# Performance work log

Measured on AMD Instinct MI355X. Metric: run time of the kernel, lower is better.

The kernel has to match this reference:

```python
import jax, jax.numpy as jnp
import numpy as np

B, S, H, NH = 4, 4096, 1024, 16
HD = H // NH  # head_dim = 64


def setup_inputs() -> dict:
    key = jax.random.key(0)
    ks = jax.random.split(key, 8)
    scale = 0.02
    return {
        "hidden_states": jax.random.normal(ks[0], (B, S, H), dtype=jnp.float32),
        "attention_mask": jnp.ones((B, S), dtype=jnp.float32),
        "Wq": jax.random.normal(ks[1], (H, H), dtype=jnp.float32) * scale,
        "bq": jnp.zeros((H,), dtype=jnp.float32),
        "Wk": jax.random.normal(ks[2], (H, H), dtype=jnp.float32) * scale,
        "bk": jnp.zeros((H,), dtype=jnp.float32),
        "Wv": jax.random.normal(ks[3], (H, H), dtype=jnp.float32) * scale,
        "bv": jnp.zeros((H,), dtype=jnp.float32),
        "Wo": jax.random.normal(ks[4], (H, H), dtype=jnp.float32) * scale,
        "bo": jnp.zeros((H,), dtype=jnp.float32),
    }


def _heads(x):
    # [B,S,H] -> [B,NH,S,HD]
    b, s, _ = x.shape
    return x.reshape(b, s, NH, HD).transpose(0, 2, 1, 3)


def reference(hidden_states, attention_mask, Wq, bq, Wk, bk, Wv, bv, Wo, bo):
    b, s, _ = hidden_states.shape
    q = _heads(hidden_states @ Wq.T + bq)
    k = _heads(hidden_states @ Wk.T + bk)
    v = _heads(hidden_states @ Wv.T + bv)

    m = attention_mask[:, None, :, None]  # [B,1,S,1]
    k = k * m
    v = v * m

    # Faithful to the torch code: kv_i = matmul(k_i[b,h,1,d], v_i[b,h,d,1])
    # is the SCALAR dot product k_t . v_t, broadcast-added to the [d,d] state.
    # => state_t = (cumsum_t k_t.v_t) * ones(d,d)
    # => o_t = state_t @ q_t = (cumsum_t k_t.v_t) * sum_j q_t[j], same for every i.
    dots = jnp.einsum('bhsd,bhsd->bhs', k, v)        # scalar k.v per step
    cum = jnp.cumsum(dots, axis=-1)                  # running state scalar
    qsum = jnp.sum(q, axis=-1)                       # [B,NH,S]
    o = jnp.broadcast_to((cum * qsum)[..., None], q.shape)  # [B,NH,S,HD]

    out = o.transpose(0, 2, 1, 3).reshape(b, s, NH * HD)
    out = out @ Wo.T + bo  # dropout is identity (eval / p handled as 0)

    # final state: last cumulative scalar broadcast over the [d,d] matrix
    state = jnp.broadcast_to(cum[:, :, -1, None, None], (b, NH, HD, HD))
    return out, state
```

## Files before the change

kernel.cpp:

```cpp
#include <hip/hip_runtime.h>


typedef __attribute__((ext_vector_type(4))) float f32x4;
typedef __attribute__((ext_vector_type(8))) short bf16x8;
typedef __attribute__((ext_vector_type(8))) unsigned short u16x8;
typedef unsigned int u32;

#define GLDS16(g, l)                                                            \
  __builtin_amdgcn_global_load_lds((const __attribute__((address_space(1))) u32*)(g), \
                                   (__attribute__((address_space(3))) u32*)(l), 16, 0, 0)
#define MFMA16(a, b, c) __builtin_amdgcn_mfma_f32_16x16x32_bf16(a, b, c, 0, 0, 0)

__device__ __forceinline__ unsigned short f2bf(float f) {
  union { float f; u32 u; } x; x.f = f;
  u32 r = (x.u + 0x7fffu + ((x.u >> 16) & 1u)) >> 16;
  return (unsigned short)r;
}

__global__ void k_prep(const float* __restrict__ X, unsigned short* __restrict__ Xb,
                       const float* __restrict__ Wq, const float* __restrict__ bq,
                       const float* __restrict__ Wk, const float* __restrict__ bk,
                       const float* __restrict__ Wv, const float* __restrict__ bv,
                       const float* __restrict__ Wo,
                       unsigned short* __restrict__ Wkb, unsigned short* __restrict__ Wvb,
                       unsigned short* __restrict__ SWb, float* __restrict__ WosT,
                       float* __restrict__ scal) {
  int blk = blockIdx.x, t = threadIdx.x;
  if (blk < 2048) {
    const float* src = (blk < 1024) ? Wk : Wv;
    unsigned short* dst = (blk < 1024) ? Wkb : Wvb;
    size_t i = ((size_t)(blk & 1023) * 256 + t) * 4;
    f32x4 v = *(const f32x4*)(src + i);
    dst[i + 0] = f2bf(v.x); dst[i + 1] = f2bf(v.y);
    dst[i + 2] = f2bf(v.z); dst[i + 3] = f2bf(v.w);
  } else if (blk < 2241) {
    int b2 = blk - 2048;
    if (b2 < 128) {
      int o = b2 * 256 + t;
      int r = o >> 10, c = o & 1023;
      float s = 0.f;
      if (r < 16) {
        for (int d = 0; d < 64; ++d) s += Wq[(size_t)(r * 64 + d) * 1024 + c];
      } else {
        int h = r - 16;
        for (int d = 0; d < 64; ++d) {
          int j = h * 64 + d;
          s += bv[j] * Wk[(size_t)j * 1024 + c] + bk[j] * Wv[(size_t)j * 1024 + c];
        }
      }
      SWb[o] = f2bf(s);
    } else if (b2 < 192) {
      int o = (b2 - 128) * 256 + t;
      int h = o >> 10, j = o & 1023;
      float s = 0.f;
      for (int d = 0; d < 64; ++d) s += Wo[(size_t)j * 1024 + h * 64 + d];
      WosT[o] = s;
    } else {
      if (t < 16) {
        float s = 0.f;
        for (int d = 0; d < 64; ++d) s += bq[t * 64 + d];
        scal[t] = s;
      } else if (t < 32) {
        int h = t - 16;
        float s = 0.f;
        for (int d = 0; d < 64; ++d) s += bk[h * 64 + d] * bv[h * 64 + d];
        scal[t] = s;
      }
    }
  } else {
    size_t i = ((size_t)(blk - 2241) * 256 + t) * 8;
    f32x4 a = *(const f32x4*)(X + i);
    f32x4 b = *(const f32x4*)(X + i + 4);
    u16x8 o;
    o[0] = f2bf(a.x); o[1] = f2bf(a.y); o[2] = f2bf(a.z); o[3] = f2bf(a.w);
    o[4] = f2bf(b.x); o[5] = f2bf(b.y); o[6] = f2bf(b.z); o[7] = f2bf(b.w);
    *(u16x8*)(Xb + i) = o;
  }
}

#define NT 32
__global__ __launch_bounds__(512, 2) void k_dualgemm(
    const unsigned short* __restrict__ Xb,
    const unsigned short* __restrict__ Wkb,
    const unsigned short* __restrict__ Wvb,
    float* __restrict__ dotsT) {
  extern __shared__ __align__(16) unsigned short lds[];
  int orig = blockIdx.x;
  int wg = (orig & 7) * 64 + (orig >> 3);
  int bx = wg & 7, by = wg >> 3;
  int row0 = by << 8, col0 = bx << 7;
  int tid = threadIdx.x, wid = tid >> 6, lane = tid & 63;
  int wrM = wid >> 1, wcN = wid & 1;
  int fr = lane & 15, fg = lane >> 4;

  int uA0 = tid, uA1 = tid + 512;
  const unsigned short* sA0 = Xb + (size_t)(row0 + (uA0 >> 2)) * 1024 + (((uA0 & 3) ^ ((uA0 >> 3) & 3)) << 3);
  const unsigned short* sA1 = Xb + (size_t)(row0 + (uA1 >> 2)) * 1024 + (((uA1 & 3) ^ ((uA1 >> 3) & 3)) << 3);
  const unsigned short* sK  = Wkb + (size_t)(col0 + (tid >> 2)) * 1024 + (((tid & 3) ^ ((tid >> 3) & 3)) << 3);
  const unsigned short* sV  = Wvb + (size_t)(col0 + (tid >> 2)) * 1024 + (((tid & 3) ^ ((tid >> 3) & 3)) << 3);
  int dA0 = wid << 9, dA1 = 4096 + (wid << 9);
  int dK = 8192 + (wid << 9), dV = 12288 + (wid << 9);

  int xsw = (fg ^ ((fr >> 1) & 3)) << 3;
  int aro = (wrM * 64 + fr) * 32 + xsw;
  int bro = (wcN * 64 + fr) * 32 + xsw;

  f32x4 ck[4][4] = {{0}}, cv[4][4] = {{0}};

#pragma unroll
  for (int p = 0; p < 3; ++p) {
    int bb = p * 16384, ko = p * 32;
    GLDS16(sA0 + ko, lds + bb + dA0);
    GLDS16(sK + ko, lds + bb + dK);
    GLDS16(sA1 + ko, lds + bb + dA1);
    GLDS16(sV + ko, lds + bb + dV);
  }

  for (int t = 0; t < NT; ++t) {
    int rb = (t & 3) << 14;
    if (t < NT - 3) { asm volatile("s_waitcnt vmcnt(8)" ::: "memory"); }
    else            { asm volatile("s_waitcnt vmcnt(0)" ::: "memory"); }
    __builtin_amdgcn_s_barrier();
    __builtin_amdgcn_sched_barrier(0);

    bf16x8 a[4], bk[4], bv[4];
#pragma unroll
    for (int mi = 0; mi < 4; ++mi) a[mi] = *(const bf16x8*)(lds + rb + aro + mi * 512);
#pragma unroll
    for (int ni = 0; ni < 2; ++ni) {
      bk[ni] = *(const bf16x8*)(lds + rb + 8192 + bro + ni * 512);
      bv[ni] = *(const bf16x8*)(lds + rb + 12288 + bro + ni * 512);
    }
    int t3 = t + 3;
    int bb = (t3 & 3) << 14, ko = t3 << 5;
    if (t3 < NT) {
      GLDS16(sA0 + ko, lds + bb + dA0);
      GLDS16(sK + ko, lds + bb + dK);
    }
    asm volatile("s_waitcnt lgkmcnt(0)" ::: "memory");
    __builtin_amdgcn_sched_barrier(0);
    __builtin_amdgcn_s_setprio(1);
#pragma unroll
    for (int mi = 0; mi < 4; ++mi)
#pragma unroll
      for (int ni = 0; ni < 2; ++ni) {
        ck[mi][ni] = MFMA16(a[mi], bk[ni], ck[mi][ni]);
        cv[mi][ni] = MFMA16(a[mi], bv[ni], cv[mi][ni]);
      }
    __builtin_amdgcn_s_setprio(0);

#pragma unroll
    for (int ni = 2; ni < 4; ++ni) {
      bk[ni] = *(const bf16x8*)(lds + rb + 8192 + bro + ni * 512);
      bv[ni] = *(const bf16x8*)(lds + rb + 12288 + bro + ni * 512);
    }
    if (t3 < NT) {
      GLDS16(sA1 + ko, lds + bb + dA1);
      GLDS16(sV + ko, lds + bb + dV);
    }
    asm volatile("s_waitcnt lgkmcnt(0)" ::: "memory");
    __builtin_amdgcn_sched_barrier(0);
    __builtin_amdgcn_s_setprio(1);
#pragma unroll
    for (int mi = 0; mi < 4; ++mi)
#pragma unroll
      for (int ni = 2; ni < 4; ++ni) {
        ck[mi][ni] = MFMA16(a[mi], bk[ni], ck[mi][ni]);
        cv[mi][ni] = MFMA16(a[mi], bv[ni], cv[mi][ni]);
      }
    __builtin_amdgcn_s_setprio(0);
  }

  float part[4][4];
#pragma unroll
  for (int mi = 0; mi < 4; ++mi)
#pragma unroll
    for (int q = 0; q < 4; ++q) {
      float s = 0.f;
#pragma unroll
      for (int ni = 0; ni < 4; ++ni) s += ck[mi][ni][q] * cv[mi][ni][q];
      part[mi][q] = s;
    }
#pragma unroll
  for (int r = 0; r < 4; ++r) {
#pragma unroll
    for (int mi = 0; mi < 4; ++mi)
#pragma unroll
      for (int q = 0; q < 4; ++q)
        part[mi][q] += __shfl_xor(part[mi][q], 1 << r, 64);
  }
  int h = bx * 2 + wcN;
  if (fr == 0) {
#pragma unroll
    for (int mi = 0; mi < 4; ++mi)
#pragma unroll
      for (int q = 0; q < 4; ++q)
        dotsT[(size_t)h * 16384 + row0 + wrM * 64 + mi * 16 + fg * 4 + q] = part[mi][q];
  }
}

__global__ __launch_bounds__(512) void k_side(const unsigned short* __restrict__ Xb,
                                              const unsigned short* __restrict__ SWb,
                                              float* __restrict__ side4) {
  __shared__ __align__(16) unsigned short As[8192];
  __shared__ __align__(16) unsigned short Ss[1024];
  int rowblk = blockIdx.x >> 2, ks = blockIdx.x & 3;
  int row0 = rowblk << 8;
  int tid = threadIdx.x, wid = tid >> 6, lane = tid & 63;
  int fr = lane & 15, fg = lane >> 4;
  int uA0 = tid, uA1 = tid + 512;
  const unsigned short* sA0 = Xb + (size_t)(row0 + (uA0 >> 2)) * 1024 + ks * 256 + (((uA0 & 3) ^ ((uA0 >> 3) & 3)) << 3);
  const unsigned short* sA1 = Xb + (size_t)(row0 + (uA1 >> 2)) * 1024 + ks * 256 + (((uA1 & 3) ^ ((uA1 >> 3) & 3)) << 3);
  int uS = ((wid & 1) << 6) + lane;
  const unsigned short* sS = SWb + (size_t)(uS >> 2) * 1024 + ks * 256 + (((uS & 3) ^ ((uS >> 3) & 3)) << 3);
  int xsw = (fg ^ ((fr >> 1) & 3)) << 3;
  int aro = (wid * 32 + fr) * 32 + xsw;
  int sro = fr * 32 + xsw;
  f32x4 acc[2][2] = {{0}};
  for (int t = 0; t < 8; ++t) {
    int ko = t << 5;
    __syncthreads();
    GLDS16(sA0 + ko, As + (wid << 9));
    GLDS16(sA1 + ko, As + 4096 + (wid << 9));
    GLDS16(sS + ko, Ss + ((wid & 1) << 9));
    __syncthreads();
    bf16x8 a0 = *(const bf16x8*)(As + aro);
    bf16x8 a1 = *(const bf16x8*)(As + aro + 512);
    bf16x8 s0 = *(const bf16x8*)(Ss + sro);
    bf16x8 s1 = *(const bf16x8*)(Ss + sro + 512);
    acc[0][0] = MFMA16(a0, s0, acc[0][0]);
    acc[0][1] = MFMA16(a0, s1, acc[0][1]);
    acc[1][0] = MFMA16(a1, s0, acc[1][0]);
    acc[1][1] = MFMA16(a1, s1, acc[1][1]);
  }
  size_t mbase = row0 + wid * 32;
#pragma unroll
  for (int mi = 0; mi < 2; ++mi)
#pragma unroll
    for (int ni = 0; ni < 2; ++ni)
#pragma unroll
      for (int q = 0; q < 4; ++q)
        side4[(size_t)((ni * 4 + ks) * 16 + fr) * 16384 + mbase + mi * 16 + fg * 4 + q] =
            acc[mi][ni][q];
}

__global__ void k_cumsum(const float* __restrict__ dotsT, const float* __restrict__ side4,
                         const float* __restrict__ scal, const float* __restrict__ mask,
                         float* __restrict__ coef, float* __restrict__ state) {
  __shared__ float csum[256];
  int b = blockIdx.x >> 4, h = blockIdx.x & 15;
  int t = threadIdx.x;
  float bqs = scal[h], dbc = scal[16 + h];
  size_t m0 = (size_t)b * 4096;
  const size_t KSS = (size_t)16 * 16384;
  const float* dro = dotsT + (size_t)h * 16384 + m0;
  const float* qb = side4 + (size_t)h * 16384 + m0;
  const float* db = side4 + 4 * KSS + (size_t)h * 16384 + m0;
  const float* mko = mask + m0;
  float loc[16], run = 0.f;
  int s0 = t * 16;
#pragma unroll
  for (int i = 0; i < 16; ++i) {
    int ii = s0 + i;
    float mk = mko[ii];
    float dball = db[ii] + db[ii + KSS] + db[ii + 2 * KSS] + db[ii + 3 * KSS];
    float d = (dro[ii] + dball + dbc) * mk * mk;
    run += d;
    loc[i] = run;
  }
  csum[t] = run;
  __syncthreads();
  for (int off = 1; off < 256; off <<= 1) {
    float v = (t >= off) ? csum[t - off] : 0.f;
    __syncthreads();
    csum[t] += v;
    __syncthreads();
  }
  float prefix = csum[t] - run;
#pragma unroll
  for (int i = 0; i < 16; ++i) {
    int ii = s0 + i;
    float cum = prefix + loc[i];
    float qs = qb[ii] + qb[ii + KSS] + qb[ii + 2 * KSS] + qb[ii + 3 * KSS];
    coef[(m0 + ii) * 16 + h] = cum * (qs + bqs);
  }
  float total = csum[255];
  float* sp = state + (size_t)(b * 16 + h) * 4096;
  for (int i = t; i < 4096; i += 256) sp[i] = total;
}

__global__ __launch_bounds__(256) void k_outgemm(const float* __restrict__ coef,
                                                 const float* __restrict__ WosT,
                                                 const float* __restrict__ bo,
                                                 float* __restrict__ out) {
  int t = threadIdx.x;
  int j0 = t * 4;
  f32x4 w4[16];
#pragma unroll
  for (int hh = 0; hh < 16; ++hh) w4[hh] = *(const f32x4*)&WosT[hh * 1024 + j0];
  f32x4 bov = *(const f32x4*)&bo[j0];
  size_t m0 = (size_t)blockIdx.x * 32;
  for (int mi = 0; mi < 32; ++mi) {
    size_t m = m0 + mi;
    const float* cm = &coef[m * 16];
    f32x4 acc = bov;
#pragma unroll
    for (int hh = 0; hh < 16; ++hh) acc += w4[hh] * cm[hh];
    *(f32x4*)&out[m * 1024 + j0] = acc;
  }
}

extern "C" void kernel_launch(void* const* d_in, const int* in_sizes, int n_in,
                              void* d_out, int out_size, void* d_ws, size_t ws_size,
                              hipStream_t stream) {
  const float* X    = (const float*)d_in[0];
  const float* mask = (const float*)d_in[1];
  const float* Wq   = (const float*)d_in[2];
  const float* bq   = (const float*)d_in[3];
  const float* Wk   = (const float*)d_in[4];
  const float* bk   = (const float*)d_in[5];
  const float* Wv   = (const float*)d_in[6];
  const float* bv   = (const float*)d_in[7];
  const float* Wo   = (const float*)d_in[8];
  const float* bo   = (const float*)d_in[9];
  float* out   = (float*)d_out;
  float* state = out + (size_t)16384 * 1024;

  char* w = (char*)d_ws;
  unsigned short* Xb  = (unsigned short*)w; w += (size_t)16384 * 1024 * 2;
  unsigned short* Wkb = (unsigned short*)w; w += (size_t)1024 * 1024 * 2;
  unsigned short* Wvb = (unsigned short*)w; w += (size_t)1024 * 1024 * 2;
  unsigned short* SWb = (unsigned short*)w; w += (size_t)32 * 1024 * 2;
  float* WosT  = (float*)w; w += (size_t)16 * 1024 * 4;
  float* scal  = (float*)w; w += 256;
  float* dotsT = (float*)w; w += (size_t)16 * 16384 * 4;
  float* side4 = (float*)w; w += (size_t)8 * 16 * 16384 * 4;
  float* coef  = (float*)w; w += (size_t)16384 * 16 * 4;

  (void)hipFuncSetAttribute((const void*)k_dualgemm,
                            hipFuncAttributeMaxDynamicSharedMemorySize, 131072);

  hipLaunchKernelGGL(k_prep,     dim3(10433), dim3(256), 0, stream,
                     X, Xb, Wq, bq, Wk, bk, Wv, bv, Wo, Wkb, Wvb, SWb, WosT, scal);
  hipLaunchKernelGGL(k_dualgemm, dim3(512),  dim3(512), 131072, stream, Xb, Wkb, Wvb, dotsT);
  hipLaunchKernelGGL(k_side,     dim3(256),  dim3(512), 0, stream, Xb, SWb, side4);
  hipLaunchKernelGGL(k_cumsum,   dim3(64),   dim3(256), 0, stream, dotsT, side4, scal,
                     mask, coef, state);
  hipLaunchKernelGGL(k_outgemm,  dim3(512),  dim3(256), 0, stream, coef, WosT, bo, out);
}
```

Measured before the change: 116.5 us.

## Merge side GEMM into dual-GEMM launch and split main loop into four phases

The separate k_side kernel is folded into k_dualgemm as 256 extra workgroups, which removes one launch and lets the side GEMM run alongside the main GEMM tail. The main K-loop is restructured into four phases (K-lo, V-lo, K-hi, V-hi), each issuing one global-to-LDS load and running its MFMAs between barriers. The goal is finer interleaving of loads with compute. The cost is many more barriers per iteration, and the side blocks now reserve 128KB of dynamic LDS, which can limit occupancy.

```diff
diff --git a/kernel.cpp b/kernel.cpp
--- a/kernel.cpp
+++ b/kernel.cpp
@@ -10,6 +10,9 @@
   __builtin_amdgcn_global_load_lds((const __attribute__((address_space(1))) u32*)(g), \
                                    (__attribute__((address_space(3))) u32*)(l), 16, 0, 0)
 #define MFMA16(a, b, c) __builtin_amdgcn_mfma_f32_16x16x32_bf16(a, b, c, 0, 0, 0)
+#define PH_BAR __builtin_amdgcn_s_barrier()
+#define LGK0 do { asm volatile("s_waitcnt lgkmcnt(0)" ::: "memory"); \
+                  __builtin_amdgcn_sched_barrier(0); } while (0)
 
 __device__ __forceinline__ unsigned short f2bf(float f) {
   union { float f; u32 u; } x; x.f = f;
@@ -83,15 +86,61 @@
     const unsigned short* __restrict__ Xb,
     const unsigned short* __restrict__ Wkb,
     const unsigned short* __restrict__ Wvb,
-    float* __restrict__ dotsT) {
+    const unsigned short* __restrict__ SWb,
+    float* __restrict__ dotsT, float* __restrict__ side4) {
   extern __shared__ __align__(16) unsigned short lds[];
   int orig = blockIdx.x;
+  int tid = threadIdx.x, wid = tid >> 6, lane = tid & 63;
+  int fr = lane & 15, fg = lane >> 4;
+
+  if (orig >= 512) {
+    int unit = orig - 512;
+    int rowblk = unit >> 2, ks = unit & 3;
+    int row0 = rowblk << 8;
+    unsigned short* As = lds;
+    unsigned short* Ss = lds + 8192;
+    int uA0 = tid, uA1 = tid + 512;
+    const unsigned short* sA0 = Xb + (size_t)(row0 + (uA0 >> 2)) * 1024 + ks * 256 + (((uA0 & 3) ^ ((uA0 >> 3) & 3)) << 3);
+    const unsigned short* sA1 = Xb + (size_t)(row0 + (uA1 >> 2)) * 1024 + ks * 256 + (((uA1 & 3) ^ ((uA1 >> 3) & 3)) << 3);
+    int uS = ((wid & 1) << 6) + lane;
+    const unsigned short* sS = SWb + (size_t)(uS >> 2) * 1024 + ks * 256 + (((uS & 3) ^ ((uS >> 3) & 3)) << 3);
+    int xsw = (fg ^ ((fr >> 1) & 3)) << 3;
+    int aro = (wid * 32 + fr) * 32 + xsw;
+    int sro = fr * 32 + xsw;
+    f32x4 acc[2][2] = {{0}};
+    for (int t = 0; t < 8; ++t) {
+      int ko = t << 5;
+      __syncthreads();
+      GLDS16(sA0 + ko, As + (wid << 9));
+      GLDS16(sA1 + ko, As + 4096 + (wid << 9));
+      GLDS16(sS + ko, Ss + ((wid & 1) << 9));
+      asm volatile("s_waitcnt vmcnt(0)" ::: "memory");
+      __syncthreads();
+      bf16x8 a0 = *(const bf16x8*)(As + aro);
+      bf16x8 a1 = *(const bf16x8*)(As + aro + 512);
+      bf16x8 s0 = *(const bf16x8*)(Ss + sro);
+      bf16x8 s1 = *(const bf16x8*)(Ss + sro + 512);
+      acc[0][0] = MFMA16(a0, s0, acc[0][0]);
+      acc[0][1] = MFMA16(a0, s1, acc[0][1]);
+      acc[1][0] = MFMA16(a1, s0, acc[1][0]);
+      acc[1][1] = MFMA16(a1, s1, acc[1][1]);
+    }
+    size_t mbase = row0 + wid * 32;
+#pragma unroll
+    for (int mi = 0; mi < 2; ++mi)
+#pragma unroll
+      for (int ni = 0; ni < 2; ++ni)
+#pragma unroll
+        for (int q = 0; q < 4; ++q)
+          side4[(size_t)((ni * 4 + ks) * 16 + fr) * 16384 + mbase + mi * 16 + fg * 4 + q] =
+              acc[mi][ni][q];
+    return;
+  }
+
   int wg = (orig & 7) * 64 + (orig >> 3);
   int bx = wg & 7, by = wg >> 3;
   int row0 = by << 8, col0 = bx << 7;
-  int tid = threadIdx.x, wid = tid >> 6, lane = tid & 63;
   int wrM = wid >> 1, wcN = wid & 1;
-  int fr = lane & 15, fg = lane >> 4;
 
   int uA0 = tid, uA1 = tid + 512;
   const unsigned short* sA0 = Xb + (size_t)(row0 + (uA0 >> 2)) * 1024 + (((uA0 & 3) ^ ((uA0 >> 3) & 3)) << 3);
@@ -115,60 +164,73 @@
     GLDS16(sA1 + ko, lds + bb + dA1);
     GLDS16(sV + ko, lds + bb + dV);
   }
+  asm volatile("s_waitcnt vmcnt(8)" ::: "memory");
+  PH_BAR;
 
   for (int t = 0; t < NT; ++t) {
-    int rb = (t & 3) << 14;
-    if (t < NT - 3) { asm volatile("s_waitcnt vmcnt(8)" ::: "memory"); }
-    else            { asm volatile("s_waitcnt vmcnt(0)" ::: "memory"); }
-    __builtin_amdgcn_s_barrier();
-    __builtin_amdgcn_sched_barrier(0);
-
+    const int rb = (t & 3) << 14;
+    const int t3 = t + 3;
+    const int bb = (t3 & 3) << 14;
+    const int ko = t3 << 5;
+    const bool st = (t3 < NT);
     bf16x8 a[4], bk[4], bv[4];
+
 #pragma unroll
     for (int mi = 0; mi < 4; ++mi) a[mi] = *(const bf16x8*)(lds + rb + aro + mi * 512);
-#pragma unroll
-    for (int ni = 0; ni < 2; ++ni) {
-      bk[ni] = *(const bf16x8*)(lds + rb + 8192 + bro + ni * 512);
-      bv[ni] = *(const bf16x8*)(lds + rb + 12288 + bro + ni * 512);
-    }
-    int t3 = t + 3;
-    int bb = (t3 & 3) << 14, ko = t3 << 5;
-    if (t3 < NT) {
-      GLDS16(sA0 + ko, lds + bb + dA0);
-      GLDS16(sK + ko, lds + bb + dK);
-    }
-    asm volatile("s_waitcnt lgkmcnt(0)" ::: "memory");
-    __builtin_amdgcn_sched_barrier(0);
+    bk[0] = *(const bf16x8*)(lds + rb + 8192 + bro);
+    bk[1] = *(const bf16x8*)(lds + rb + 8192 + bro + 512);
+    if (st) GLDS16(sA0 + ko, lds + bb + dA0);
+    PH_BAR; LGK0;
     __builtin_amdgcn_s_setprio(1);
 #pragma unroll
-    for (int mi = 0; mi < 4; ++mi)
-#pragma unroll
-      for (int ni = 0; ni < 2; ++ni) {
-        ck[mi][ni] = MFMA16(a[mi], bk[ni], ck[mi][ni]);
-        cv[mi][ni] = MFMA16(a[mi], bv[ni], cv[mi][ni]);
-      }
+    for (int mi = 0; mi < 4; ++mi) {
+      ck[mi][0] = MFMA16(a[mi], bk[0], ck[mi][0]);
+      ck[mi][1] = MFMA16(a[mi], bk[1], ck[mi][1]);
+    }
     __builtin_amdgcn_s_setprio(0);
-
-#pragma unroll
-    for (int ni = 2; ni < 4; ++ni) {
-      bk[ni] = *(const bf16x8*)(lds + rb + 8192 + bro + ni * 512);
-      bv[ni] = *(const bf16x8*)(lds + rb + 12288 + bro + ni * 512);
-    }
-    if (t3 < NT) {
-      GLDS16(sA1 + ko, lds + bb + dA1);
-      GLDS16(sV + ko, lds + bb + dV);
-    }
-    asm volatile("s_waitcnt lgkmcnt(0)" ::: "memory");
-    __builtin_amdgcn_sched_barrier(0);
+    PH_BAR;
+
+    bv[0] = *(const bf16x8*)(lds + rb + 12288 + bro);
+    bv[1] = *(const bf16x8*)(lds + rb + 12288 + bro + 512);
+    if (st) GLDS16(sK + ko, lds + bb + dK);
+    PH_BAR; LGK0;
     __builtin_amdgcn_s_setprio(1);
 #pragma unroll
-    for (int mi = 0; mi < 4; ++mi)
-#pragma unroll
-      for (int ni = 2; ni < 4; ++ni) {
-        ck[mi][ni] = MFMA16(a[mi], bk[ni], ck[mi][ni]);
-        cv[mi][ni] = MFMA16(a[mi], bv[ni], cv[mi][ni]);
-      }
+    for (int mi = 0; mi < 4; ++mi) {
+      cv[mi][0] = MFMA16(a[mi], bv[0], cv[mi][0]);
+      cv[mi][1] = MFMA16(a[mi], bv[1], cv[mi][1]);
+    }
     __builtin_amdgcn_s_setprio(0);
+    PH_BAR;
+
+    bk[2] = *(const bf16x8*)(lds + rb + 8192 + bro + 1024);
+    bk[3] = *(const bf16x8*)(lds + rb + 8192 + bro + 1536);
+    if (st) GLDS16(sA1 + ko, lds + bb + dA1);
+    PH_BAR; LGK0;
+    __builtin_amdgcn_s_setprio(1);
+#pragma unroll
+    for (int mi = 0; mi < 4; ++mi) {
+      ck[mi][2] = MFMA16(a[mi], bk[2], ck[mi][2]);
+      ck[mi][3] = MFMA16(a[mi], bk[3], ck[mi][3]);
+    }
+    __builtin_amdgcn_s_setprio(0);
+    PH_BAR;
+
+    bv[2] = *(const bf16x8*)(lds + rb + 12288 + bro + 1024);
+    bv[3] = *(const bf16x8*)(lds + rb + 12288 + bro + 1536);
+    if (st) GLDS16(sV + ko, lds + bb + dV);
+    PH_BAR; LGK0;
+    __builtin_amdgcn_s_setprio(1);
+#pragma unroll
+    for (int mi = 0; mi < 4; ++mi) {
+      cv[mi][2] = MFMA16(a[mi], bv[2], cv[mi][2]);
+      cv[mi][3] = MFMA16(a[mi], bv[3], cv[mi][3]);
+    }
+    __builtin_amdgcn_s_setprio(0);
+    if (t <= NT - 4)      { asm volatile("s_waitcnt vmcnt(8)" ::: "memory"); }
+    else if (t == NT - 3) { asm volatile("s_waitcnt vmcnt(4)" ::: "memory"); }
+    else                  { asm volatile("s_waitcnt vmcnt(0)" ::: "memory"); }
+    PH_BAR;
   }
 
   float part[4][4];
@@ -197,51 +259,6 @@
       for (int q = 0; q < 4; ++q)
         dotsT[(size_t)h * 16384 + row0 + wrM * 64 + mi * 16 + fg * 4 + q] = part[mi][q];
   }
-}
-
-__global__ __launch_bounds__(512) void k_side(const unsigned short* __restrict__ Xb,
-                                              const unsigned short* __restrict__ SWb,
-                                              float* __restrict__ side4) {
-  __shared__ __align__(16) unsigned short As[8192];
-  __shared__ __align__(16) unsigned short Ss[1024];
-  int rowblk = blockIdx.x >> 2, ks = blockIdx.x & 3;
-  int row0 = rowblk << 8;
-  int tid = threadIdx.x, wid = tid >> 6, lane = tid & 63;
-  int fr = lane & 15, fg = lane >> 4;
-  int uA0 = tid, uA1 = tid + 512;
-  const unsigned short* sA0 = Xb + (size_t)(row0 + (uA0 >> 2)) * 1024 + ks * 256 + (((uA0 & 3) ^ ((uA0 >> 3) & 3)) << 3);
-  const unsigned short* sA1 = Xb + (size_t)(row0 + (uA1 >> 2)) * 1024 + ks * 256 + (((uA1 & 3) ^ ((uA1 >> 3) & 3)) << 3);
-  int uS = ((wid & 1) << 6) + lane;
-  const unsigned short* sS = SWb + (size_t)(uS >> 2) * 1024 + ks * 256 + (((uS & 3) ^ ((uS >> 3) & 3)) << 3);
-  int xsw = (fg ^ ((fr >> 1) & 3)) << 3;
-  int aro = (wid * 32 + fr) * 32 + xsw;
-  int sro = fr * 32 + xsw;
-  f32x4 acc[2][2] = {{0}};
-  for (int t = 0; t < 8; ++t) {
-    int ko = t << 5;
-    __syncthreads();
-    GLDS16(sA0 + ko, As + (wid << 9));
-    GLDS16(sA1 + ko, As + 4096 + (wid << 9));
-    GLDS16(sS + ko, Ss + ((wid & 1) << 9));
-    __syncthreads();
-    bf16x8 a0 = *(const bf16x8*)(As + aro);
-    bf16x8 a1 = *(const bf16x8*)(As + aro + 512);
-    bf16x8 s0 = *(const bf16x8*)(Ss + sro);
-    bf16x8 s1 = *(const bf16x8*)(Ss + sro + 512);
-    acc[0][0] = MFMA16(a0, s0, acc[0][0]);
-    acc[0][1] = MFMA16(a0, s1, acc[0][1]);
-    acc[1][0] = MFMA16(a1, s0, acc[1][0]);
-    acc[1][1] = MFMA16(a1, s1, acc[1][1]);
-  }
-  size_t mbase = row0 + wid * 32;
-#pragma unroll
-  for (int mi = 0; mi < 2; ++mi)
-#pragma unroll
-    for (int ni = 0; ni < 2; ++ni)
-#pragma unroll
-      for (int q = 0; q < 4; ++q)
-        side4[(size_t)((ni * 4 + ks) * 16 + fr) * 16384 + mbase + mi * 16 + fg * 4 + q] =
-            acc[mi][ni][q];
 }
 
 __global__ void k_cumsum(const float* __restrict__ dotsT, const float* __restrict__ side4,
@@ -342,8 +359,8 @@
 
   hipLaunchKernelGGL(k_prep,     dim3(10433), dim3(256), 0, stream,
                      X, Xb, Wq, bq, Wk, bk, Wv, bv, Wo, Wkb, Wvb, SWb, WosT, scal);
-  hipLaunchKernelGGL(k_dualgemm, dim3(512),  dim3(512), 131072, stream, Xb, Wkb, Wvb, dotsT);
-  hipLaunchKernelGGL(k_side,     dim3(256),  dim3(512), 0, stream, Xb, SWb, side4);
+  hipLaunchKernelGGL(k_dualgemm, dim3(768),  dim3(512), 131072, stream, Xb, Wkb, Wvb, SWb,
+                     dotsT, side4);
   hipLaunchKernelGGL(k_cumsum,   dim3(64),   dim3(256), 0, stream, dotsT, side4, scal,
                      mask, coef, state);
   hipLaunchKernelGGL(k_outgemm,  dim3(512),  dim3(256), 0, stream, coef, WosT, bo, out);
```

New measurement: 122.0 us. +4.8%, slower.

## Fuse side q-sum/bias-dot GEMM into dual GEMM and restructure phase barriers

Applied to the files above, without the earlier changes.

Removes the separate k_side kernel by having the column-block-0 workgroups of k_dualgemm also stage the small SWb weight slice in LDS and accumulate the q-sum and bias-dot projections with extra MFMAs. The LDS buffer grows per stage and launch bounds drop to one block per CU. The main loop now splits into a K phase and a V phase separated by explicit barriers, with the vmcnt wait moved to the end of each iteration. k_cumsum now reads one finished partial per quantity instead of summing four split-K partials. The risks are lower occupancy and load imbalance, because the bx==0 blocks do extra work.

```diff
diff --git a/kernel.cpp b/kernel.cpp
--- a/kernel.cpp
+++ b/kernel.cpp
@@ -10,6 +10,9 @@
   __builtin_amdgcn_global_load_lds((const __attribute__((address_space(1))) u32*)(g), \
                                    (__attribute__((address_space(3))) u32*)(l), 16, 0, 0)
 #define MFMA16(a, b, c) __builtin_amdgcn_mfma_f32_16x16x32_bf16(a, b, c, 0, 0, 0)
+#define PH_BAR __builtin_amdgcn_s_barrier()
+#define LGK0 do { asm volatile("s_waitcnt lgkmcnt(0)" ::: "memory"); \
+                  __builtin_amdgcn_sched_barrier(0); } while (0)
 
 __device__ __forceinline__ unsigned short f2bf(float f) {
   union { float f; u32 u; } x; x.f = f;
@@ -79,11 +82,13 @@
 }
 
 #define NT 32
-__global__ __launch_bounds__(512, 2) void k_dualgemm(
+#define BUFS 17408
+__global__ __launch_bounds__(512, 1) void k_dualgemm(
     const unsigned short* __restrict__ Xb,
     const unsigned short* __restrict__ Wkb,
     const unsigned short* __restrict__ Wvb,
-    float* __restrict__ dotsT) {
+    const unsigned short* __restrict__ SWb,
+    float* __restrict__ dotsT, float* __restrict__ qsumT, float* __restrict__ dotbT) {
   extern __shared__ __align__(16) unsigned short lds[];
   int orig = blockIdx.x;
   int wg = (orig & 7) * 64 + (orig >> 3);
@@ -92,83 +97,90 @@
   int tid = threadIdx.x, wid = tid >> 6, lane = tid & 63;
   int wrM = wid >> 1, wcN = wid & 1;
   int fr = lane & 15, fg = lane >> 4;
+  bool side = (bx == 0);
 
   int uA0 = tid, uA1 = tid + 512;
   const unsigned short* sA0 = Xb + (size_t)(row0 + (uA0 >> 2)) * 1024 + (((uA0 & 3) ^ ((uA0 >> 3) & 3)) << 3);
   const unsigned short* sA1 = Xb + (size_t)(row0 + (uA1 >> 2)) * 1024 + (((uA1 & 3) ^ ((uA1 >> 3) & 3)) << 3);
   const unsigned short* sK  = Wkb + (size_t)(col0 + (tid >> 2)) * 1024 + (((tid & 3) ^ ((tid >> 3) & 3)) << 3);
   const unsigned short* sV  = Wvb + (size_t)(col0 + (tid >> 2)) * 1024 + (((tid & 3) ^ ((tid >> 3) & 3)) << 3);
+  const unsigned short* sS  = SWb + (size_t)(tid >> 2) * 1024 + (((tid & 3) ^ ((tid >> 3) & 3)) << 3);
   int dA0 = wid << 9, dA1 = 4096 + (wid << 9);
   int dK = 8192 + (wid << 9), dV = 12288 + (wid << 9);
+  int dS = 16384 + (wid << 9);
+  bool stageSW = side && (wid < 2);
 
   int xsw = (fg ^ ((fr >> 1) & 3)) << 3;
   int aro = (wrM * 64 + fr) * 32 + xsw;
   int bro = (wcN * 64 + fr) * 32 + xsw;
+  int swo = 16384 + (wcN * 16 + fr) * 32 + xsw;
 
   f32x4 ck[4][4] = {{0}}, cv[4][4] = {{0}};
+  f32x4 qa[4] = {0, 0, 0, 0};
 
 #pragma unroll
   for (int p = 0; p < 3; ++p) {
-    int bb = p * 16384, ko = p * 32;
+    int bb = p * BUFS, ko = p * 32;
     GLDS16(sA0 + ko, lds + bb + dA0);
     GLDS16(sK + ko, lds + bb + dK);
     GLDS16(sA1 + ko, lds + bb + dA1);
     GLDS16(sV + ko, lds + bb + dV);
-  }
+    if (stageSW) GLDS16(sS + ko, lds + bb + dS);
+  }
+  asm volatile("s_waitcnt vmcnt(8)" ::: "memory");
+  PH_BAR;
 
   for (int t = 0; t < NT; ++t) {
-    int rb = (t & 3) << 14;
-    if (t < NT - 3) { asm volatile("s_waitcnt vmcnt(8)" ::: "memory"); }
-    else            { asm volatile("s_waitcnt vmcnt(0)" ::: "memory"); }
-    __builtin_amdgcn_s_barrier();
-    __builtin_amdgcn_sched_barrier(0);
-
+    const int rb = (t & 3) * BUFS;
+    const int t3 = t + 3;
+    const int bb = (t3 & 3) * BUFS;
+    const int ko = t3 << 5;
+    const bool st = (t3 < NT);
     bf16x8 a[4], bk[4], bv[4];
+
 #pragma unroll
     for (int mi = 0; mi < 4; ++mi) a[mi] = *(const bf16x8*)(lds + rb + aro + mi * 512);
 #pragma unroll
-    for (int ni = 0; ni < 2; ++ni) {
-      bk[ni] = *(const bf16x8*)(lds + rb + 8192 + bro + ni * 512);
-      bv[ni] = *(const bf16x8*)(lds + rb + 12288 + bro + ni * 512);
-    }
-    int t3 = t + 3;
-    int bb = (t3 & 3) << 14, ko = t3 << 5;
-    if (t3 < NT) {
+    for (int ni = 0; ni < 4; ++ni) bk[ni] = *(const bf16x8*)(lds + rb + 8192 + bro + ni * 512);
+    if (st) {
       GLDS16(sA0 + ko, lds + bb + dA0);
       GLDS16(sK + ko, lds + bb + dK);
     }
-    asm volatile("s_waitcnt lgkmcnt(0)" ::: "memory");
-    __builtin_amdgcn_sched_barrier(0);
+    PH_BAR; LGK0;
     __builtin_amdgcn_s_setprio(1);
 #pragma unroll
     for (int mi = 0; mi < 4; ++mi)
 #pragma unroll
-      for (int ni = 0; ni < 2; ++ni) {
+      for (int ni = 0; ni < 4; ++ni)
         ck[mi][ni] = MFMA16(a[mi], bk[ni], ck[mi][ni]);
-        cv[mi][ni] = MFMA16(a[mi], bv[ni], cv[mi][ni]);
-      }
     __builtin_amdgcn_s_setprio(0);
-
-#pragma unroll
-    for (int ni = 2; ni < 4; ++ni) {
-      bk[ni] = *(const bf16x8*)(lds + rb + 8192 + bro + ni * 512);
-      bv[ni] = *(const bf16x8*)(lds + rb + 12288 + bro + ni * 512);
-    }
-    if (t3 < NT) {
+    PH_BAR;
+
+#pragma unroll
+    for (int ni = 0; ni < 4; ++ni) bv[ni] = *(const bf16x8*)(lds + rb + 12288 + bro + ni * 512);
+    bf16x8 sw;
+    if (side) sw = *(const bf16x8*)(lds + rb + swo);
+    if (st) {
       GLDS16(sA1 + ko, lds + bb + dA1);
       GLDS16(sV + ko, lds + bb + dV);
-    }
-    asm volatile("s_waitcnt lgkmcnt(0)" ::: "memory");
-    __builtin_amdgcn_sched_barrier(0);
+      if (stageSW) GLDS16(sS + ko, lds + bb + dS);
+    }
+    PH_BAR; LGK0;
     __builtin_amdgcn_s_setprio(1);
 #pragma unroll
     for (int mi = 0; mi < 4; ++mi)
 #pragma unroll
-      for (int ni = 2; ni < 4; ++ni) {
-        ck[mi][ni] = MFMA16(a[mi], bk[ni], ck[mi][ni]);
+      for (int ni = 0; ni < 4; ++ni)
         cv[mi][ni] = MFMA16(a[mi], bv[ni], cv[mi][ni]);
-      }
+    if (side) {
+#pragma unroll
+      for (int mi = 0; mi < 4; ++mi) qa[mi] = MFMA16(a[mi], sw, qa[mi]);
+    }
     __builtin_amdgcn_s_setprio(0);
+    if (t <= NT - 4)      { asm volatile("s_waitcnt vmcnt(8)" ::: "memory"); }
+    else if (t == NT - 3) { asm volatile("s_waitcnt vmcnt(4)" ::: "memory"); }
+    else                  { asm volatile("s_waitcnt vmcnt(0)" ::: "memory"); }
+    PH_BAR;
   }
 
   float part[4][4];
@@ -197,65 +209,28 @@
       for (int q = 0; q < 4; ++q)
         dotsT[(size_t)h * 16384 + row0 + wrM * 64 + mi * 16 + fg * 4 + q] = part[mi][q];
   }
-}
-
-__global__ __launch_bounds__(512) void k_side(const unsigned short* __restrict__ Xb,
-                                              const unsigned short* __restrict__ SWb,
-                                              float* __restrict__ side4) {
-  __shared__ __align__(16) unsigned short As[8192];
-  __shared__ __align__(16) unsigned short Ss[1024];
-  int rowblk = blockIdx.x >> 2, ks = blockIdx.x & 3;
-  int row0 = rowblk << 8;
-  int tid = threadIdx.x, wid = tid >> 6, lane = tid & 63;
-  int fr = lane & 15, fg = lane >> 4;
-  int uA0 = tid, uA1 = tid + 512;
-  const unsigned short* sA0 = Xb + (size_t)(row0 + (uA0 >> 2)) * 1024 + ks * 256 + (((uA0 & 3) ^ ((uA0 >> 3) & 3)) << 3);
-  const unsigned short* sA1 = Xb + (size_t)(row0 + (uA1 >> 2)) * 1024 + ks * 256 + (((uA1 & 3) ^ ((uA1 >> 3) & 3)) << 3);
-  int uS = ((wid & 1) << 6) + lane;
-  const unsigned short* sS = SWb + (size_t)(uS >> 2) * 1024 + ks * 256 + (((uS & 3) ^ ((uS >> 3) & 3)) << 3);
-  int xsw = (fg ^ ((fr >> 1) & 3)) << 3;
-  int aro = (wid * 32 + fr) * 32 + xsw;
-  int sro = fr * 32 + xsw;
-  f32x4 acc[2][2] = {{0}};
-  for (int t = 0; t < 8; ++t) {
-    int ko = t << 5;
-    __syncthreads();
-    GLDS16(sA0 + ko, As + (wid << 9));
-    GLDS16(sA1 + ko, As + 4096 + (wid << 9));
-    GLDS16(sS + ko, Ss + ((wid & 1) << 9));
-    __syncthreads();
-    bf16x8 a0 = *(const bf16x8*)(As + aro);
-    bf16x8 a1 = *(const bf16x8*)(As + aro + 512);
-    bf16x8 s0 = *(const bf16x8*)(Ss + sro);
-    bf16x8 s1 = *(const bf16x8*)(Ss + sro + 512);
-    acc[0][0] = MFMA16(a0, s0, acc[0][0]);
-    acc[0][1] = MFMA16(a0, s1, acc[0][1]);
-    acc[1][0] = MFMA16(a1, s0, acc[1][0]);
-    acc[1][1] = MFMA16(a1, s1, acc[1][1]);
-  }
-  size_t mbase = row0 + wid * 32;
-#pragma unroll
-  for (int mi = 0; mi < 2; ++mi)
-#pragma unroll
-    for (int ni = 0; ni < 2; ++ni)
+  if (side) {
+    float* dst = (wcN == 0) ? qsumT : dotbT;
+#pragma unroll
+    for (int mi = 0; mi < 4; ++mi)
 #pragma unroll
       for (int q = 0; q < 4; ++q)
-        side4[(size_t)((ni * 4 + ks) * 16 + fr) * 16384 + mbase + mi * 16 + fg * 4 + q] =
-            acc[mi][ni][q];
-}
-
-__global__ void k_cumsum(const float* __restrict__ dotsT, const float* __restrict__ side4,
-                         const float* __restrict__ scal, const float* __restrict__ mask,
+        dst[(size_t)fr * 16384 + row0 + wrM * 64 + mi * 16 + fg * 4 + q] = qa[mi][q];
+  }
+}
+
+__global__ void k_cumsum(const float* __restrict__ dotsT, const float* __restrict__ dotbT,
+                         const float* __restrict__ qsumT, const float* __restrict__ scal,
+                         const float* __restrict__ mask,
                          float* __restrict__ coef, float* __restrict__ state) {
   __shared__ float csum[256];
   int b = blockIdx.x >> 4, h = blockIdx.x & 15;
   int t = threadIdx.x;
   float bqs = scal[h], dbc = scal[16 + h];
   size_t m0 = (size_t)b * 4096;
-  const size_t KSS = (size_t)16 * 16384;
   const float* dro = dotsT + (size_t)h * 16384 + m0;
-  const float* qb = side4 + (size_t)h * 16384 + m0;
-  const float* db = side4 + 4 * KSS + (size_t)h * 16384 + m0;
+  const float* dbo = dotbT + (size_t)h * 16384 + m0;
+  const float* qso = qsumT + (size_t)h * 16384 + m0;
   const float* mko = mask + m0;
   float loc[16], run = 0.f;
   int s0 = t * 16;
@@ -263,8 +238,7 @@
   for (int i = 0; i < 16; ++i) {
     int ii = s0 + i;
     float mk = mko[ii];
-    float dball = db[ii] + db[ii + KSS] + db[ii + 2 * KSS] + db[ii + 3 * KSS];
-    float d = (dro[ii] + dball + dbc) * mk * mk;
+    float d = (dro[ii] + dbo[ii] + dbc) * mk * mk;
     run += d;
     loc[i] = run;
   }
@@ -281,8 +255,7 @@
   for (int i = 0; i < 16; ++i) {
     int ii = s0 + i;
     float cum = prefix + loc[i];
-    float qs = qb[ii] + qb[ii + KSS] + qb[ii + 2 * KSS] + qb[ii + 3 * KSS];
-    coef[(m0 + ii) * 16 + h] = cum * (qs + bqs);
+    coef[(m0 + ii) * 16 + h] = cum * (qso[ii] + bqs);
   }
   float total = csum[255];
   float* sp = state + (size_t)(b * 16 + h) * 4096;
@@ -334,17 +307,18 @@
   float* WosT  = (float*)w; w += (size_t)16 * 1024 * 4;
   float* scal  = (float*)w; w += 256;
   float* dotsT = (float*)w; w += (size_t)16 * 16384 * 4;
-  float* side4 = (float*)w; w += (size_t)8 * 16 * 16384 * 4;
+  float* qsumT = (float*)w; w += (size_t)16 * 16384 * 4;
+  float* dotbT = (float*)w; w += (size_t)16 * 16384 * 4;
   float* coef  = (float*)w; w += (size_t)16384 * 16 * 4;
 
   (void)hipFuncSetAttribute((const void*)k_dualgemm,
-                            hipFuncAttributeMaxDynamicSharedMemorySize, 131072);
+                            hipFuncAttributeMaxDynamicSharedMemorySize, 139264);
 
   hipLaunchKernelGGL(k_prep,     dim3(10433), dim3(256), 0, stream,
                      X, Xb, Wq, bq, Wk, bk, Wv, bv, Wo, Wkb, Wvb, SWb, WosT, scal);
-  hipLaunchKernelGGL(k_dualgemm, dim3(512),  dim3(512), 131072, stream, Xb, Wkb, Wvb, dotsT);
-  hipLaunchKernelGGL(k_side,     dim3(256),  dim3(512), 0, stream, Xb, SWb, side4);
-  hipLaunchKernelGGL(k_cumsum,   dim3(64),   dim3(256), 0, stream, dotsT, side4, scal,
+  hipLaunchKernelGGL(k_dualgemm, dim3(512),  dim3(512), 139264, stream, Xb, Wkb, Wvb, SWb,
+                     dotsT, qsumT, dotbT);
+  hipLaunchKernelGGL(k_cumsum,   dim3(64),   dim3(256), 0, stream, dotsT, dotbT, qsumT, scal,
                      mask, coef, state);
   hipLaunchKernelGGL(k_outgemm,  dim3(512),  dim3(256), 0, stream, coef, WosT, bo, out);
 }
```

Measured after the change: 116.1 us. About the same (-0.3%).

## Merge side GEMM into dual GEMM launch as extra blocks, relax LDS waits

Applied to the files above, without the earlier changes.

Folds the k_side kernel into k_dualgemm by launching 256 extra blocks that take the side-projection path, so both GEMMs run in one grid and one launch gap disappears. It also drops the explicit lgkmcnt waits and sched_barriers in the main loop, leaving the compiler to schedule LDS reads against MFMAs. The side blocks now ask for the full 128KB of dynamic LDS, which limits how many of them fit on a CU. Without the manual waits, the compiler's scheduling may be worse than the hand-placed version.

```diff
diff --git a/kernel.cpp b/kernel.cpp
--- a/kernel.cpp
+++ b/kernel.cpp
@@ -79,19 +79,66 @@
 }
 
 #define NT 32
+#define BUFS 16384
 __global__ __launch_bounds__(512, 2) void k_dualgemm(
     const unsigned short* __restrict__ Xb,
     const unsigned short* __restrict__ Wkb,
     const unsigned short* __restrict__ Wvb,
-    float* __restrict__ dotsT) {
+    const unsigned short* __restrict__ SWb,
+    float* __restrict__ dotsT, float* __restrict__ side4) {
   extern __shared__ __align__(16) unsigned short lds[];
   int orig = blockIdx.x;
+  int tid = threadIdx.x, wid = tid >> 6, lane = tid & 63;
+  int fr = lane & 15, fg = lane >> 4;
+
+  if (orig >= 512) {
+    int unit = orig - 512;
+    int rowblk = unit >> 2, ks = unit & 3;
+    int row0 = rowblk << 8;
+    unsigned short* As = lds;
+    unsigned short* Ss = lds + 8192;
+    int uA0 = tid, uA1 = tid + 512;
+    const unsigned short* sA0 = Xb + (size_t)(row0 + (uA0 >> 2)) * 1024 + ks * 256 + (((uA0 & 3) ^ ((uA0 >> 3) & 3)) << 3);
+    const unsigned short* sA1 = Xb + (size_t)(row0 + (uA1 >> 2)) * 1024 + ks * 256 + (((uA1 & 3) ^ ((uA1 >> 3) & 3)) << 3);
+    int uS = ((wid & 1) << 6) + lane;
+    const unsigned short* sS = SWb + (size_t)(uS >> 2) * 1024 + ks * 256 + (((uS & 3) ^ ((uS >> 3) & 3)) << 3);
+    int xsw = (fg ^ ((fr >> 1) & 3)) << 3;
+    int aro = (wid * 32 + fr) * 32 + xsw;
+    int sro = fr * 32 + xsw;
+    f32x4 acc[2][2] = {{0}};
+    for (int t = 0; t < 8; ++t) {
+      int ko = t << 5;
+      __syncthreads();
+      GLDS16(sA0 + ko, As + (wid << 9));
+      GLDS16(sA1 + ko, As + 4096 + (wid << 9));
+      if (wid < 2) GLDS16(sS + ko, Ss + ((wid & 1) << 9));
+      asm volatile("s_waitcnt vmcnt(0)" ::: "memory");
+      __syncthreads();
+      bf16x8 a0 = *(const bf16x8*)(As + aro);
+      bf16x8 a1 = *(const bf16x8*)(As + aro + 512);
+      bf16x8 s0 = *(const bf16x8*)(Ss + sro);
+      bf16x8 s1 = *(const bf16x8*)(Ss + sro + 512);
+      acc[0][0] = MFMA16(a0, s0, acc[0][0]);
+      acc[0][1] = MFMA16(a0, s1, acc[0][1]);
+      acc[1][0] = MFMA16(a1, s0, acc[1][0]);
+      acc[1][1] = MFMA16(a1, s1, acc[1][1]);
+    }
+    size_t mbase = row0 + wid * 32;
+#pragma unroll
+    for (int mi = 0; mi < 2; ++mi)
+#pragma unroll
+      for (int ni = 0; ni < 2; ++ni)
+#pragma unroll
+        for (int q = 0; q < 4; ++q)
+          side4[(size_t)((ni * 4 + ks) * 16 + fr) * 16384 + mbase + mi * 16 + fg * 4 + q] =
+              acc[mi][ni][q];
+    return;
+  }
+
   int wg = (orig & 7) * 64 + (orig >> 3);
   int bx = wg & 7, by = wg >> 3;
   int row0 = by << 8, col0 = bx << 7;
-  int tid = threadIdx.x, wid = tid >> 6, lane = tid & 63;
   int wrM = wid >> 1, wcN = wid & 1;
-  int fr = lane & 15, fg = lane >> 4;
 
   int uA0 = tid, uA1 = tid + 512;
   const unsigned short* sA0 = Xb + (size_t)(row0 + (uA0 >> 2)) * 1024 + (((uA0 & 3) ^ ((uA0 >> 3) & 3)) << 3);
@@ -109,7 +156,7 @@
 
 #pragma unroll
   for (int p = 0; p < 3; ++p) {
-    int bb = p * 16384, ko = p * 32;
+    int bb = p * BUFS, ko = p * 32;
     GLDS16(sA0 + ko, lds + bb + dA0);
     GLDS16(sK + ko, lds + bb + dK);
     GLDS16(sA1 + ko, lds + bb + dA1);
@@ -117,11 +164,10 @@
   }
 
   for (int t = 0; t < NT; ++t) {
-    int rb = (t & 3) << 14;
+    int rb = (t & 3) * BUFS;
     if (t < NT - 3) { asm volatile("s_waitcnt vmcnt(8)" ::: "memory"); }
     else            { asm volatile("s_waitcnt vmcnt(0)" ::: "memory"); }
     __builtin_amdgcn_s_barrier();
-    __builtin_amdgcn_sched_barrier(0);
 
     bf16x8 a[4], bk[4], bv[4];
 #pragma unroll
@@ -132,13 +178,11 @@
       bv[ni] = *(const bf16x8*)(lds + rb + 12288 + bro + ni * 512);
     }
     int t3 = t + 3;
-    int bb = (t3 & 3) << 14, ko = t3 << 5;
+    int bb = (t3 & 3) * BUFS, ko = t3 << 5;
     if (t3 < NT) {
       GLDS16(sA0 + ko, lds + bb + dA0);
       GLDS16(sK + ko, lds + bb + dK);
     }
-    asm volatile("s_waitcnt lgkmcnt(0)" ::: "memory");
-    __builtin_amdgcn_sched_barrier(0);
     __builtin_amdgcn_s_setprio(1);
 #pragma unroll
     for (int mi = 0; mi < 4; ++mi)
@@ -158,8 +202,6 @@
       GLDS16(sA1 + ko, lds + bb + dA1);
       GLDS16(sV + ko, lds + bb + dV);
     }
-    asm volatile("s_waitcnt lgkmcnt(0)" ::: "memory");
-    __builtin_amdgcn_sched_barrier(0);
     __builtin_amdgcn_s_setprio(1);
 #pragma unroll
     for (int mi = 0; mi < 4; ++mi)
@@ -197,51 +239,6 @@
       for (int q = 0; q < 4; ++q)
         dotsT[(size_t)h * 16384 + row0 + wrM * 64 + mi * 16 + fg * 4 + q] = part[mi][q];
   }
-}
-
-__global__ __launch_bounds__(512) void k_side(const unsigned short* __restrict__ Xb,
-                                              const unsigned short* __restrict__ SWb,
-                                              float* __restrict__ side4) {
-  __shared__ __align__(16) unsigned short As[8192];
-  __shared__ __align__(16) unsigned short Ss[1024];
-  int rowblk = blockIdx.x >> 2, ks = blockIdx.x & 3;
-  int row0 = rowblk << 8;
-  int tid = threadIdx.x, wid = tid >> 6, lane = tid & 63;
-  int fr = lane & 15, fg = lane >> 4;
-  int uA0 = tid, uA1 = tid + 512;
-  const unsigned short* sA0 = Xb + (size_t)(row0 + (uA0 >> 2)) * 1024 + ks * 256 + (((uA0 & 3) ^ ((uA0 >> 3) & 3)) << 3);
-  const unsigned short* sA1 = Xb + (size_t)(row0 + (uA1 >> 2)) * 1024 + ks * 256 + (((uA1 & 3) ^ ((uA1 >> 3) & 3)) << 3);
-  int uS = ((wid & 1) << 6) + lane;
-  const unsigned short* sS = SWb + (size_t)(uS >> 2) * 1024 + ks * 256 + (((uS & 3) ^ ((uS >> 3) & 3)) << 3);
-  int xsw = (fg ^ ((fr >> 1) & 3)) << 3;
-  int aro = (wid * 32 + fr) * 32 + xsw;
-  int sro = fr * 32 + xsw;
-  f32x4 acc[2][2] = {{0}};
-  for (int t = 0; t < 8; ++t) {
-    int ko = t << 5;
-    __syncthreads();
-    GLDS16(sA0 + ko, As + (wid << 9));
-    GLDS16(sA1 + ko, As + 4096 + (wid << 9));
-    GLDS16(sS + ko, Ss + ((wid & 1) << 9));
-    __syncthreads();
-    bf16x8 a0 = *(const bf16x8*)(As + aro);
-    bf16x8 a1 = *(const bf16x8*)(As + aro + 512);
-    bf16x8 s0 = *(const bf16x8*)(Ss + sro);
-    bf16x8 s1 = *(const bf16x8*)(Ss + sro + 512);
-    acc[0][0] = MFMA16(a0, s0, acc[0][0]);
-    acc[0][1] = MFMA16(a0, s1, acc[0][1]);
-    acc[1][0] = MFMA16(a1, s0, acc[1][0]);
-    acc[1][1] = MFMA16(a1, s1, acc[1][1]);
-  }
-  size_t mbase = row0 + wid * 32;
-#pragma unroll
-  for (int mi = 0; mi < 2; ++mi)
-#pragma unroll
-    for (int ni = 0; ni < 2; ++ni)
-#pragma unroll
-      for (int q = 0; q < 4; ++q)
-        side4[(size_t)((ni * 4 + ks) * 16 + fr) * 16384 + mbase + mi * 16 + fg * 4 + q] =
-            acc[mi][ni][q];
 }
 
 __global__ void k_cumsum(const float* __restrict__ dotsT, const float* __restrict__ side4,
@@ -342,8 +339,8 @@
 
   hipLaunchKernelGGL(k_prep,     dim3(10433), dim3(256), 0, stream,
                      X, Xb, Wq, bq, Wk, bk, Wv, bv, Wo, Wkb, Wvb, SWb, WosT, scal);
-  hipLaunchKernelGGL(k_dualgemm, dim3(512),  dim3(512), 131072, stream, Xb, Wkb, Wvb, dotsT);
-  hipLaunchKernelGGL(k_side,     dim3(256),  dim3(512), 0, stream, Xb, SWb, side4);
+  hipLaunchKernelGGL(k_dualgemm, dim3(768),  dim3(512), 131072, stream, Xb, Wkb, Wvb, SWb,
+                     dotsT, side4);
   hipLaunchKernelGGL(k_cumsum,   dim3(64),   dim3(256), 0, stream, dotsT, side4, scal,
                      mask, coef, state);
   hipLaunchKernelGGL(k_outgemm,  dim3(512),  dim3(256), 0, stream, coef, WosT, bo, out);
```

New measurement: 113.2 us. 2.8% less time.
